# Performance work log

Hardware: AMD Instinct MI355X
Metric: run time of the kernel (lower is better)

Reference implementation:

```python
import jax, jax.numpy as jnp
import numpy as np

N_NODES = 50000
N_EDGES = 1600000
D_IN = 512
D_HEAD = 64
N_HEADS_L1 = 4


def _segment_mean(data, seg_ids, num_segments, counts):
    s = jax.ops.segment_sum(data, seg_ids, num_segments=num_segments)
    denom = jnp.maximum(counts, 1.0)
    return jnp.where(counts[:, None] > 0, s / denom[:, None], 0.0)


def setup_inputs() -> dict:
    key = jax.random.key(0)
    k1, k2, k3, k4 = jax.random.split(key, 4)
    node_features = jax.random.normal(k1, (N_NODES, D_IN), dtype=jnp.float32)
    edge_index = jax.random.randint(k2, (2, N_EDGES), 0, N_NODES, dtype=jnp.int32)
    W1 = jax.random.normal(k3, (N_HEADS_L1, D_IN, D_HEAD), dtype=jnp.float32) * (1.0 / np.sqrt(D_IN))
    W2 = jax.random.normal(k4, (N_HEADS_L1 * D_HEAD, D_HEAD), dtype=jnp.float32) * (1.0 / np.sqrt(N_HEADS_L1 * D_HEAD))
    return {"node_features": node_features, "edge_index": edge_index, "W1": W1, "W2": W2}


def reference(node_features, edge_index, W1, W2):
    n = node_features.shape[0]
    src = edge_index[0]  # segment ids (destination of aggregation in TF code)
    dst = edge_index[1]  # gathered neighbors
    counts = jax.ops.segment_sum(jnp.ones_like(src, dtype=node_features.dtype), src, num_segments=n)

    # Layer 1: 4 heads, Dense(64, no bias) -> gather(dst) -> unsorted_segment_mean(src) -> concat -> elu
    head_outs = []
    for i in range(N_HEADS_L1):
        t = node_features @ W1[i]                 # (N, 64)
        agg = _segment_mean(t[dst], src, n, counts)  # (N, 64)
        head_outs.append(agg)
    h = jax.nn.elu(jnp.concatenate(head_outs, axis=-1))  # (N, 256)

    # Layer 2: 1 head, linear activation
    t2 = h @ W2                                   # (N, 64)
    out = _segment_mean(t2[dst], src, n, counts)  # (N, 64)
    return out
```

## Files before the change

kernel.cpp:

```cpp
#include <hip/hip_runtime.h>
#include <hip/hip_bf16.h>
#include <stdint.h>

#define N_NODES 50000
#define N_EDGES 1600000
#define D_IN    512
#define D_H1    256
#define D_OUT   64

#define NBUK    196
#define MAXB    9216
#define EPB     4096
#define NPB     391
#define SLOT    96

#define NR      50001
#define ZROW    50000

typedef __attribute__((ext_vector_type(8))) short  short8;
typedef __attribute__((ext_vector_type(4))) float  f32x4;
typedef __attribute__((ext_vector_type(2))) float  f32x2;
typedef __attribute__((ext_vector_type(4))) unsigned int u32x4;
typedef __attribute__((ext_vector_type(2))) unsigned int u32x2;

typedef __attribute__((address_space(1))) void GASV;
typedef __attribute__((address_space(3))) void LASV;

static __device__ __forceinline__ unsigned short f2bf(float f) {
    union { float f; unsigned int u; } c; c.f = f;
    unsigned int u = c.u;
    return (unsigned short)((u + 0x7FFFu + ((u >> 16) & 1u)) >> 16);
}
static __device__ __forceinline__ unsigned int cvtpk(float a, float b) {
    unsigned int r;
    asm("v_cvt_pk_bf16_f32 %0, %1, %2" : "=v"(r) : "v"(a), "v"(b));
    return r;
}
static __device__ __forceinline__ unsigned short f2bf1(float f) {
    return (unsigned short)cvtpk(f, f);
}
static __device__ __forceinline__ float uasf(unsigned int u) {
    union { unsigned int u; float f; } c; c.u = u; return c.f;
}

static __device__ __forceinline__ void waitvm(int n) {
    switch (n) {
    case 0: asm volatile("s_waitcnt vmcnt(0)" ::: "memory"); break;
    case 1: asm volatile("s_waitcnt vmcnt(1)" ::: "memory"); break;
    case 2: asm volatile("s_waitcnt vmcnt(2)" ::: "memory"); break;
    case 3: asm volatile("s_waitcnt vmcnt(3)" ::: "memory"); break;
    case 4: asm volatile("s_waitcnt vmcnt(4)" ::: "memory"); break;
    case 5: asm volatile("s_waitcnt vmcnt(5)" ::: "memory"); break;
    case 6: asm volatile("s_waitcnt vmcnt(6)" ::: "memory"); break;
    default: asm volatile("s_waitcnt vmcnt(7)" ::: "memory"); break;
    }
    __builtin_amdgcn_sched_barrier(0);
}


__global__ __launch_bounds__(256) void part_kernel(const int* __restrict__ src,
                                                   const int* __restrict__ dst,
                                                   int* __restrict__ gcnt,
                                                   unsigned int* __restrict__ gbuk) {
    __shared__ int hist[NBUK];
    __shared__ int lofs[NBUK];
    __shared__ int gbase[NBUK];
    __shared__ int sbuf[256];
    __shared__ unsigned int sorted[EPB];
    __shared__ unsigned char bid[EPB];

    const int t  = threadIdx.x;
    const int e0 = blockIdx.x * EPB;
    int ec = N_EDGES - e0; if (ec > EPB) ec = EPB;

    for (int i = t; i < NBUK; i += 256) hist[i] = 0;
    __syncthreads();

    unsigned int rec[16];
    int bb[16], idx[16];
#pragma unroll
    for (int j = 0; j < 16; ++j) {
        int i = j * 256 + t;
        if (i < ec) {
            int s = src[e0 + i], d = dst[e0 + i];
            int b = s >> 8;
            rec[j] = ((unsigned int)(s & 255) << 16) | (unsigned int)d;
            bb[j]  = b;
            idx[j] = atomicAdd(&hist[b], 1);
        } else bb[j] = -1;
    }
    __syncthreads();

    int v = (t < NBUK) ? hist[t] : 0;
    sbuf[t] = v;
    __syncthreads();
#pragma unroll
    for (int off = 1; off < 256; off <<= 1) {
        int x = (t >= off) ? sbuf[t - off] : 0;
        __syncthreads();
        sbuf[t] += x;
        __syncthreads();
    }
    if (t < NBUK) {
        lofs[t]  = sbuf[t] - v;
        gbase[t] = atomicAdd(&gcnt[t], v);
    }
    __syncthreads();

#pragma unroll
    for (int j = 0; j < 16; ++j) {
        if (bb[j] >= 0) {
            int p = lofs[bb[j]] + idx[j];
            sorted[p] = rec[j];
            bid[p] = (unsigned char)bb[j];
        }
    }
    __syncthreads();

    for (int i = t; i < ec; i += 256) {
        int b = bid[i];
        int p = gbase[b] + (i - lofs[b]);
        gbuk[(size_t)b * MAXB + p] = sorted[i];
    }
}


__global__ __launch_bounds__(256) void sort_kernel(const int* __restrict__ gcnt,
                                                   const unsigned int* __restrict__ gbuk,
                                                   unsigned short* __restrict__ sdst,
                                                   int* __restrict__ deg) {
    __shared__ int hist[256];
    __shared__ int nofs[256];
    __shared__ int sbuf[256];
    __shared__ unsigned short list[MAXB];

    const int t = threadIdx.x;
    const int b = blockIdx.x;
    const int cnt = gcnt[b];
    const unsigned int* buk = gbuk + (size_t)b * MAXB;

    hist[t] = 0;
    __syncthreads();
    for (int i = t; i < cnt; i += 256)
        atomicAdd(&hist[buk[i] >> 16], 1);
    __syncthreads();

    int v = hist[t];
    sbuf[t] = v;
    __syncthreads();
#pragma unroll
    for (int off = 1; off < 256; off <<= 1) {
        int x = (t >= off) ? sbuf[t - off] : 0;
        __syncthreads();
        sbuf[t] += x;
        __syncthreads();
    }
    nofs[t] = sbuf[t] - v;
    const int n = b * 256 + t;
    if (n < N_NODES) deg[n] = v;
    __syncthreads();

    for (int i = t; i < cnt; i += 256) {
        unsigned int r = buk[i];
        int p = atomicAdd(&nofs[r >> 16], 1);
        list[p] = (unsigned short)(r & 0xffffu);
    }
    __syncthreads();

    for (int base = 0; base < 256; base += 32) {
        int node = base + (t >> 3);
        int l8   = t & 7;
        int vv   = hist[node];
        int beg  = nofs[node] - vv;
        int n2   = b * 256 + node;
        if (n2 < N_NODES) {
            int words = ((vv + 3) & ~3) >> 1;
            unsigned int* out32 = (unsigned int*)(sdst + (size_t)n2 * SLOT);
            for (int j2 = l8; j2 < words; j2 += 8) {
                unsigned int lo = (2 * j2     < vv) ? list[beg + 2 * j2]     : (unsigned int)ZROW;
                unsigned int hi = (2 * j2 + 1 < vv) ? list[beg + 2 * j2 + 1] : (unsigned int)ZROW;
                out32[j2] = lo | (hi << 16);
            }
        }
    }
}


__global__ void convw_kernel(const float* __restrict__ W1, const float* __restrict__ W2,
                             unsigned short* __restrict__ Bt1, unsigned short* __restrict__ Bt2,
                             unsigned short* __restrict__ t1, unsigned short* __restrict__ t2) {
    int i = blockIdx.x * 256 + threadIdx.x;
    if (i < 4 * 512 * 64) {
        int h = i >> 15;
        int k = (i >> 6) & 511;
        int j = i & 63;
        Bt1[(h * 64 + j) * 512 + k] = f2bf(W1[i]);
    } else if (i < 4 * 512 * 64 + 256 * 64) {
        int r = i - 4 * 512 * 64;
        int k = r >> 6;
        int n = r & 63;
        Bt2[n * 256 + k] = f2bf(W2[r]);
    } else {
        int r = i - (4 * 512 * 64 + 256 * 64);
        if (r < 8 * 32) {
            t1[(size_t)(r >> 5) * ((size_t)NR * 32) + (size_t)ZROW * 32 + (r & 31)] = 0;
        } else if (r < 8 * 32 + 2 * 32) {
            int q = r - 8 * 32;
            t2[(size_t)(q >> 5) * ((size_t)NR * 32) + (size_t)ZROW * 32 + (q & 31)] = 0;
        }
    }
}


__global__ __launch_bounds__(512) void gemm1_kernel(const float* __restrict__ A,
                                                    const unsigned short* __restrict__ Bt,
                                                    unsigned short* __restrict__ C) {
    constexpr int BM = 128, BK = 32, LDK = 40, K = D_IN, M = N_NODES;
    __shared__ unsigned short As[BM * LDK];
    __shared__ unsigned short Bs[256 * LDK];

    const int tid  = threadIdx.x;
    const int lane = tid & 63;
    const int w    = tid >> 6;
    const int wm   = (w >> 2) * 64;
    const int wn   = (w & 3) * 64;
    const int quad = lane >> 4;
    const int l15  = lane & 15;
    const int bm   = blockIdx.x;

    f32x4 acc[4][4];
#pragma unroll
    for (int mi = 0; mi < 4; ++mi)
#pragma unroll
        for (int ni = 0; ni < 4; ++ni)
            acc[mi][ni] = (f32x4){0.f, 0.f, 0.f, 0.f};

    const int r0 = tid >> 2;
    const int f8 = tid & 3;

    for (int k0 = 0; k0 < K; k0 += BK) {
        {
            int grow = bm * BM + r0;
            if (grow >= M) grow = M - 1;
            const float* ap = A + (size_t)grow * K + k0 + f8 * 8;
            f32x4 v0 = *(const f32x4*)ap;
            f32x4 v1 = *(const f32x4*)(ap + 4);
            u32x4 pk;
            pk[0] = cvtpk(v0[0], v0[1]);
            pk[1] = cvtpk(v0[2], v0[3]);
            pk[2] = cvtpk(v1[0], v1[1]);
            pk[3] = cvtpk(v1[2], v1[3]);
            *(u32x4*)&As[r0 * LDK + f8 * 8] = pk;
        }
        {
#pragma unroll
            for (int p = 0; p < 2; ++p) {
                int row = p * 128 + r0;
                u32x4 v = *(const u32x4*)(Bt + (size_t)row * K + k0 + f8 * 8);
                *(u32x4*)&Bs[row * LDK + f8 * 8] = v;
            }
        }
        __syncthreads();

        short8 af[4], bfr[4];
#pragma unroll
        for (int mi = 0; mi < 4; ++mi)
            af[mi] = *(const short8*)&As[(wm + mi * 16 + l15) * LDK + quad * 8];
#pragma unroll
        for (int ni = 0; ni < 4; ++ni)
            bfr[ni] = *(const short8*)&Bs[(wn + ni * 16 + l15) * LDK + quad * 8];
#pragma unroll
        for (int mi = 0; mi < 4; ++mi)
#pragma unroll
            for (int ni = 0; ni < 4; ++ni)
                acc[mi][ni] = __builtin_amdgcn_mfma_f32_16x16x32_bf16(af[mi], bfr[ni], acc[mi][ni], 0, 0, 0);
        __syncthreads();
    }

#pragma unroll
    for (int mi = 0; mi < 4; ++mi) {
        int row0 = bm * BM + wm + mi * 16 + quad * 4;
#pragma unroll
        for (int ni = 0; ni < 4; ++ni) {
            int col = wn + ni * 16 + l15;
            unsigned short* cp = C + (size_t)(col >> 5) * ((size_t)NR * 32) + (col & 31);
#pragma unroll
            for (int r = 0; r < 4; ++r) {
                int row = row0 + r;
                if (row < M) cp[(size_t)row * 32] = f2bf1(acc[mi][ni][r]);
            }
        }
    }
}


__global__ __launch_bounds__(256) void gemm2_kernel(const unsigned short* __restrict__ A,
                                                    const unsigned short* __restrict__ Bt,
                                                    unsigned short* __restrict__ C) {
    constexpr int BM = 64, BK = 32, LDK = 40, K = D_H1, M = N_NODES;
    __shared__ unsigned short As[BM * LDK];
    __shared__ unsigned short Bs[64 * LDK];

    const int tid  = threadIdx.x;
    const int lane = tid & 63;
    const int w    = tid >> 6;
    const int wm   = (w >> 1) * 32;
    const int wn   = (w & 1) * 32;
    const int quad = lane >> 4;
    const int l15  = lane & 15;
    const int bm   = blockIdx.x;

    f32x4 acc[2][2];
#pragma unroll
    for (int mi = 0; mi < 2; ++mi)
#pragma unroll
        for (int ni = 0; ni < 2; ++ni)
            acc[mi][ni] = (f32x4){0.f, 0.f, 0.f, 0.f};

    for (int k0 = 0; k0 < K; k0 += BK) {
        {
            int f8 = tid & 3;
            int r0 = tid >> 2;
            int grow = bm * BM + r0;
            if (grow >= M) grow = M - 1;
            u32x4 v = *(const u32x4*)(A + (size_t)grow * K + k0 + f8 * 8);
            *(u32x4*)&As[r0 * LDK + f8 * 8] = v;
        }
        {
            int f8 = tid & 3;
            int r0 = tid >> 2;
            u32x4 v = *(const u32x4*)(Bt + (size_t)r0 * K + k0 + f8 * 8);
            *(u32x4*)&Bs[r0 * LDK + f8 * 8] = v;
        }
        __syncthreads();

        short8 af[2], bfr[2];
#pragma unroll
        for (int mi = 0; mi < 2; ++mi)
            af[mi] = *(const short8*)&As[(wm + mi * 16 + l15) * LDK + quad * 8];
#pragma unroll
        for (int ni = 0; ni < 2; ++ni)
            bfr[ni] = *(const short8*)&Bs[(wn + ni * 16 + l15) * LDK + quad * 8];
#pragma unroll
        for (int mi = 0; mi < 2; ++mi)
#pragma unroll
            for (int ni = 0; ni < 2; ++ni)
                acc[mi][ni] = __builtin_amdgcn_mfma_f32_16x16x32_bf16(af[mi], bfr[ni], acc[mi][ni], 0, 0, 0);
        __syncthreads();
    }

#pragma unroll
    for (int mi = 0; mi < 2; ++mi) {
        int row0 = bm * BM + wm + mi * 16 + quad * 4;
#pragma unroll
        for (int ni = 0; ni < 2; ++ni) {
            int col = wn + ni * 16 + l15;
            unsigned short* cp = C + (size_t)(col >> 5) * ((size_t)NR * 32) + (col & 31);
#pragma unroll
            for (int r = 0; r < 4; ++r) {
                int row = row0 + r;
                if (row < M) cp[(size_t)row * 32] = f2bf1(acc[mi][ni][r]);
            }
        }
    }
}


#define AGG_ISSUE(J, B, NJ)                                                             \
    int NJ;                                                                             \
    {                                                                                   \
        const int nq4   = (end##J + 3) >> 2;                       \
        const int nfull = nq4 >> 2;                         \
        const int tq    = nq4 & 3;                               \
        int r16[4];                                                                     \
        _Pragma("unroll")                                                               \
        for (int k = 0; k < 4; ++k)                                                     \
            r16[k] = __shfl(elv##J, ((k << 4) + (lane >> 2)) & 63);                     \
        const int rtail = __shfl(elv##J, ((nfull << 4) + (lane >> 2)) & 63);            \
        for (int k = 0; k < nfull; ++k)                                                 \
            __builtin_amdgcn_global_load_lds(                                           \
                (GASV*)(tb32 + ((unsigned)r16[k] << 4) + ((lane & 3) << 2)),            \
                (LASV*)(&ring[w][B][k << 8]), 16, 0, 0);                                \
        if (lane < (tq << 4))                                                           \
            __builtin_amdgcn_global_load_lds(                                           \
                (GASV*)(tb32 + ((unsigned)rtail << 4) + ((lane & 3) << 2)),             \
                (LASV*)(&ring[w][B][nfull << 8]), 16, 0, 0);                            \
        NJ = nfull + (tq ? 1 : 0);                                                      \
    }

#define AGG_CONSUME(J, B)                                                               \
    {                                                                                   \
        const int nq = (end##J + 3) >> 2;                                               \
        f32x2 Acc = {0.f, 0.f};                                                         \
        const unsigned int* rb = &ring[w][B][lane];                                     \
        for (int q = 0; q < nq; ++q) {                                                  \
            unsigned int v = rb[q << 6];                                                \
            Acc.x += uasf(v << 16);                                                     \
            Acc.y += uasf(v & 0xffff0000u);                                             \
        }                                                                               \
        f32x2 Bv;                                                                       \
        Bv.x = __shfl_xor(Acc.x, 16); Bv.y = __shfl_xor(Acc.y, 16); Acc += Bv;          \
        Bv.x = __shfl_xor(Acc.x, 32); Bv.y = __shfl_xor(Acc.y, 32); Acc += Bv;          \
        if (lane < 16) {                                                                \
            float iv = (end##J > 0) ? (1.0f / (float)end##J) : 0.f;                     \
            float m0 = Acc.x * iv, m1 = Acc.y * iv;                                     \
            if (ELU) {                                                                  \
                m0 = (m0 > 0.f) ? m0 : (__expf(m0) - 1.f);                              \
                m1 = (m1 > 0.f) ? m1 : (__expf(m1) - 1.f);                              \
                *(unsigned int*)&hout[(size_t)(s0 + J) * D_H1 + slice * 32 + (lane & 15) * 2] = cvtpk(m0, m1); \
            } else {                                                                    \
                f32x2 r; r.x = m0; r.y = m1;                                            \
                *(f32x2*)(fout + (size_t)(s0 + J) * D_OUT + slice * 32 + (lane & 15) * 2) = r; \
            }                                                                           \
        }                                                                               \
        __builtin_amdgcn_sched_barrier(0);                                              \
    }

template<int LOGS, bool ELU>
__global__ __launch_bounds__(256) void agg_kernel(const unsigned short* __restrict__ t,
                                                  const int* __restrict__ deg,
                                                  const unsigned short* __restrict__ sdst,
                                                  unsigned short* __restrict__ hout,
                                                  float* __restrict__ fout) {
    __shared__ __align__(16) unsigned int ring[4][2][1024];
    const int bi    = blockIdx.x;
    const int slice = bi & ((1 << LOGS) - 1);
    const int g     = bi >> LOGS;
    const int w     = __builtin_amdgcn_readfirstlane(threadIdx.x >> 6);
    const int lane  = threadIdx.x & 63;
    const unsigned int* tb32 = (const unsigned int*)t + (size_t)slice * ((size_t)NR * 16);

    const int s0 = g * 16 + w * 4;
    const int end0 = deg[s0 + 0], end1 = deg[s0 + 1], end2 = deg[s0 + 2], end3 = deg[s0 + 3];
    const int elv0 = sdst[(size_t)(s0 + 0) * SLOT + lane];
    const int elv1 = sdst[(size_t)(s0 + 1) * SLOT + lane];
    const int elv2 = sdst[(size_t)(s0 + 2) * SLOT + lane];
    const int elv3 = sdst[(size_t)(s0 + 3) * SLOT + lane];

    AGG_ISSUE(0, 0, n0i);
    AGG_ISSUE(1, 1, n1i); waitvm(n1i);
    AGG_CONSUME(0, 0);
    AGG_ISSUE(2, 0, n2i); waitvm(n2i + 1);
    AGG_CONSUME(1, 1);
    AGG_ISSUE(3, 1, n3i); waitvm(n3i + 1);
    AGG_CONSUME(2, 0);
    waitvm(1);
    AGG_CONSUME(3, 1);
}


extern "C" void kernel_launch(void* const* d_in, const int* in_sizes, int n_in,
                              void* d_out, int out_size, void* d_ws, size_t ws_size,
                              hipStream_t stream) {
    const float* X  = (const float*)d_in[0];
    const int*   ei = (const int*)d_in[1];
    const float* W1 = (const float*)d_in[2];
    const float* W2 = (const float*)d_in[3];
    const int* src = ei;
    const int* dst = ei + N_EDGES;

    char* ws = (char*)d_ws;
    size_t off = 0;
    auto alloc = [&](size_t bytes) {
        off = (off + 255) & ~(size_t)255;
        void* p = ws + off;
        off += bytes;
        return p;
    };
    int*          gcnt = (int*)alloc((size_t)NBUK * 4);
    unsigned int* gbuk = (unsigned int*)alloc((size_t)NBUK * MAXB * 4);
    unsigned short* sdst = (unsigned short*)alloc(((size_t)N_NODES * SLOT + 64) * 2);
    int*          deg  = (int*)alloc((size_t)N_NODES * 4);
    unsigned short* Bt1 = (unsigned short*)alloc((size_t)D_H1 * D_IN * 2);
    unsigned short* Bt2 = (unsigned short*)alloc((size_t)D_OUT * D_H1 * 2);
    unsigned short* t1  = (unsigned short*)alloc((size_t)8 * NR * 32 * 2);
    unsigned short* h   = (unsigned short*)alloc((size_t)N_NODES * D_H1 * 2);
    unsigned short* t2  = (unsigned short*)alloc((size_t)2 * NR * 32 * 2);

    hipMemsetAsync(gcnt, 0, (size_t)NBUK * 4, stream);

    part_kernel<<<NPB, 256, 0, stream>>>(src, dst, gcnt, gbuk);
    sort_kernel<<<NBUK, 256, 0, stream>>>(gcnt, gbuk, sdst, deg);
    convw_kernel<<<(4 * 512 * 64 + 256 * 64 + 8 * 32 + 2 * 32 + 255) / 256, 256, 0, stream>>>(
        W1, W2, Bt1, Bt2, t1, t2);

    gemm1_kernel<<<(N_NODES + 127) / 128, 512, 0, stream>>>(X, Bt1, t1);
    agg_kernel<3, true><<<(N_NODES / 16) * 8, 256, 0, stream>>>(t1, deg, sdst, h, nullptr);
    gemm2_kernel<<<(N_NODES + 63) / 64, 256, 0, stream>>>(h, Bt2, t2);
    agg_kernel<1, false><<<(N_NODES / 16) * 2, 256, 0, stream>>>(t2, deg, sdst, nullptr, (float*)d_out);
}
```

Baseline: 370.5 us.

## Fuse layer-1 aggregation with layer-2 GEMM and switch to row-major t1/t2

Replaces the sliced column-major t1/t2 layout with row-major rows, so each gathered neighbour row is one contiguous 512-byte (t1) or 128-byte (t2) load. A new aggf kernel averages a whole 256-wide row per node, applies ELU, keeps h in LDS and multiplies it by W2 with MFMA in the same block. This removes the h round trip and the separate gemm2 launch. Layer-2 aggregation gets its own kernel with a chunked double-buffered pipeline, and sdst padding is rounded up to multiples of 8 so those chunks are full. In exchange the whole neighbour loop runs serially in fewer blocks with a deeper per-node pipeline, which may lower occupancy and latency hiding.

```diff
diff --git a/kernel.cpp b/kernel.cpp
--- a/kernel.cpp
+++ b/kernel.cpp
@@ -42,19 +42,8 @@
 static __device__ __forceinline__ float uasf(unsigned int u) {
     union { unsigned int u; float f; } c; c.u = u; return c.f;
 }
-
-static __device__ __forceinline__ void waitvm(int n) {
-    switch (n) {
-    case 0: asm volatile("s_waitcnt vmcnt(0)" ::: "memory"); break;
-    case 1: asm volatile("s_waitcnt vmcnt(1)" ::: "memory"); break;
-    case 2: asm volatile("s_waitcnt vmcnt(2)" ::: "memory"); break;
-    case 3: asm volatile("s_waitcnt vmcnt(3)" ::: "memory"); break;
-    case 4: asm volatile("s_waitcnt vmcnt(4)" ::: "memory"); break;
-    case 5: asm volatile("s_waitcnt vmcnt(5)" ::: "memory"); break;
-    case 6: asm volatile("s_waitcnt vmcnt(6)" ::: "memory"); break;
-    default: asm volatile("s_waitcnt vmcnt(7)" ::: "memory"); break;
-    }
-    __builtin_amdgcn_sched_barrier(0);
+static __device__ __forceinline__ void glds16(const unsigned int* g, unsigned int* l) {
+    __builtin_amdgcn_global_load_lds((GASV*)g, (LASV*)l, 16, 0, 0);
 }
 
 
@@ -174,7 +163,7 @@
         int beg  = nofs[node] - vv;
         int n2   = b * 256 + node;
         if (n2 < N_NODES) {
-            int words = ((vv + 3) & ~3) >> 1;
+            int words = ((vv + 7) & ~7) >> 1;
             unsigned int* out32 = (unsigned int*)(sdst + (size_t)n2 * SLOT);
             for (int j2 = l8; j2 < words; j2 += 8) {
                 unsigned int lo = (2 * j2     < vv) ? list[beg + 2 * j2]     : (unsigned int)ZROW;
@@ -202,11 +191,10 @@
         Bt2[n * 256 + k] = f2bf(W2[r]);
     } else {
         int r = i - (4 * 512 * 64 + 256 * 64);
-        if (r < 8 * 32) {
-            t1[(size_t)(r >> 5) * ((size_t)NR * 32) + (size_t)ZROW * 32 + (r & 31)] = 0;
-        } else if (r < 8 * 32 + 2 * 32) {
-            int q = r - 8 * 32;
-            t2[(size_t)(q >> 5) * ((size_t)NR * 32) + (size_t)ZROW * 32 + (q & 31)] = 0;
+        if (r < 256) {
+            t1[(size_t)ZROW * 256 + r] = 0;
+        } else if (r < 256 + 64) {
+            t2[(size_t)ZROW * 64 + (r - 256)] = 0;
         }
     }
 }
@@ -283,169 +271,182 @@
 #pragma unroll
         for (int ni = 0; ni < 4; ++ni) {
             int col = wn + ni * 16 + l15;
-            unsigned short* cp = C + (size_t)(col >> 5) * ((size_t)NR * 32) + (col & 31);
 #pragma unroll
             for (int r = 0; r < 4; ++r) {
                 int row = row0 + r;
-                if (row < M) cp[(size_t)row * 32] = f2bf1(acc[mi][ni][r]);
+                if (row < M) C[(size_t)row * 256 + col] = f2bf1(acc[mi][ni][r]);
             }
         }
     }
 }
 
 
-__global__ __launch_bounds__(256) void gemm2_kernel(const unsigned short* __restrict__ A,
-                                                    const unsigned short* __restrict__ Bt,
-                                                    unsigned short* __restrict__ C) {
-    constexpr int BM = 64, BK = 32, LDK = 40, K = D_H1, M = N_NODES;
-    __shared__ unsigned short As[BM * LDK];
-    __shared__ unsigned short Bs[64 * LDK];
-
-    const int tid  = threadIdx.x;
-    const int lane = tid & 63;
-    const int w    = tid >> 6;
-    const int wm   = (w >> 1) * 32;
-    const int wn   = (w & 1) * 32;
-    const int quad = lane >> 4;
-    const int l15  = lane & 15;
-    const int bm   = blockIdx.x;
-
-    f32x4 acc[2][2];
-#pragma unroll
-    for (int mi = 0; mi < 2; ++mi)
-#pragma unroll
-        for (int ni = 0; ni < 2; ++ni)
-            acc[mi][ni] = (f32x4){0.f, 0.f, 0.f, 0.f};
-
-    for (int k0 = 0; k0 < K; k0 += BK) {
-        {
-            int f8 = tid & 3;
-            int r0 = tid >> 2;
-            int grow = bm * BM + r0;
-            if (grow >= M) grow = M - 1;
-            u32x4 v = *(const u32x4*)(A + (size_t)grow * K + k0 + f8 * 8);
-            *(u32x4*)&As[r0 * LDK + f8 * 8] = v;
-        }
-        {
-            int f8 = tid & 3;
-            int r0 = tid >> 2;
-            u32x4 v = *(const u32x4*)(Bt + (size_t)r0 * K + k0 + f8 * 8);
-            *(u32x4*)&Bs[r0 * LDK + f8 * 8] = v;
-        }
-        __syncthreads();
-
-        short8 af[2], bfr[2];
-#pragma unroll
-        for (int mi = 0; mi < 2; ++mi)
-            af[mi] = *(const short8*)&As[(wm + mi * 16 + l15) * LDK + quad * 8];
-#pragma unroll
-        for (int ni = 0; ni < 2; ++ni)
-            bfr[ni] = *(const short8*)&Bs[(wn + ni * 16 + l15) * LDK + quad * 8];
-#pragma unroll
-        for (int mi = 0; mi < 2; ++mi)
-#pragma unroll
-            for (int ni = 0; ni < 2; ++ni)
-                acc[mi][ni] = __builtin_amdgcn_mfma_f32_16x16x32_bf16(af[mi], bfr[ni], acc[mi][ni], 0, 0, 0);
-        __syncthreads();
-    }
-
-#pragma unroll
-    for (int mi = 0; mi < 2; ++mi) {
-        int row0 = bm * BM + wm + mi * 16 + quad * 4;
-#pragma unroll
-        for (int ni = 0; ni < 2; ++ni) {
-            int col = wn + ni * 16 + l15;
-            unsigned short* cp = C + (size_t)(col >> 5) * ((size_t)NR * 32) + (col & 31);
-#pragma unroll
-            for (int r = 0; r < 4; ++r) {
-                int row = row0 + r;
-                if (row < M) cp[(size_t)row * 32] = f2bf1(acc[mi][ni][r]);
-            }
-        }
-    }
-}
-
-
-#define AGG_ISSUE(J, B, NJ)                                                             \
-    int NJ;                                                                             \
-    {                                                                                   \
-        const int nq4   = (end##J + 3) >> 2;                       \
-        const int nfull = nq4 >> 2;                         \
-        const int tq    = nq4 & 3;                               \
-        int r16[4];                                                                     \
-        _Pragma("unroll")                                                               \
-        for (int k = 0; k < 4; ++k)                                                     \
-            r16[k] = __shfl(elv##J, ((k << 4) + (lane >> 2)) & 63);                     \
-        const int rtail = __shfl(elv##J, ((nfull << 4) + (lane >> 2)) & 63);            \
-        for (int k = 0; k < nfull; ++k)                                                 \
-            __builtin_amdgcn_global_load_lds(                                           \
-                (GASV*)(tb32 + ((unsigned)r16[k] << 4) + ((lane & 3) << 2)),            \
-                (LASV*)(&ring[w][B][k << 8]), 16, 0, 0);                                \
-        if (lane < (tq << 4))                                                           \
-            __builtin_amdgcn_global_load_lds(                                           \
-                (GASV*)(tb32 + ((unsigned)rtail << 4) + ((lane & 3) << 2)),             \
-                (LASV*)(&ring[w][B][nfull << 8]), 16, 0, 0);                            \
-        NJ = nfull + (tq ? 1 : 0);                                                      \
-    }
-
-#define AGG_CONSUME(J, B)                                                               \
-    {                                                                                   \
-        const int nq = (end##J + 3) >> 2;                                               \
-        f32x2 Acc = {0.f, 0.f};                                                         \
-        const unsigned int* rb = &ring[w][B][lane];                                     \
-        for (int q = 0; q < nq; ++q) {                                                  \
-            unsigned int v = rb[q << 6];                                                \
-            Acc.x += uasf(v << 16);                                                     \
-            Acc.y += uasf(v & 0xffff0000u);                                             \
-        }                                                                               \
-        f32x2 Bv;                                                                       \
-        Bv.x = __shfl_xor(Acc.x, 16); Bv.y = __shfl_xor(Acc.y, 16); Acc += Bv;          \
-        Bv.x = __shfl_xor(Acc.x, 32); Bv.y = __shfl_xor(Acc.y, 32); Acc += Bv;          \
-        if (lane < 16) {                                                                \
-            float iv = (end##J > 0) ? (1.0f / (float)end##J) : 0.f;                     \
-            float m0 = Acc.x * iv, m1 = Acc.y * iv;                                     \
-            if (ELU) {                                                                  \
-                m0 = (m0 > 0.f) ? m0 : (__expf(m0) - 1.f);                              \
-                m1 = (m1 > 0.f) ? m1 : (__expf(m1) - 1.f);                              \
-                *(unsigned int*)&hout[(size_t)(s0 + J) * D_H1 + slice * 32 + (lane & 15) * 2] = cvtpk(m0, m1); \
-            } else {                                                                    \
-                f32x2 r; r.x = m0; r.y = m1;                                            \
-                *(f32x2*)(fout + (size_t)(s0 + J) * D_OUT + slice * 32 + (lane & 15) * 2) = r; \
-            }                                                                           \
-        }                                                                               \
-        __builtin_amdgcn_sched_barrier(0);                                              \
-    }
-
-template<int LOGS, bool ELU>
-__global__ __launch_bounds__(256) void agg_kernel(const unsigned short* __restrict__ t,
-                                                  const int* __restrict__ deg,
-                                                  const unsigned short* __restrict__ sdst,
-                                                  unsigned short* __restrict__ hout,
-                                                  float* __restrict__ fout) {
+__global__ __launch_bounds__(256) void aggf_kernel(const unsigned short* __restrict__ t1,
+                                                   const int* __restrict__ deg,
+                                                   const unsigned short* __restrict__ sdst,
+                                                   const unsigned short* __restrict__ Bt2,
+                                                   unsigned short* __restrict__ t2) {
     __shared__ __align__(16) unsigned int ring[4][2][1024];
-    const int bi    = blockIdx.x;
-    const int slice = bi & ((1 << LOGS) - 1);
-    const int g     = bi >> LOGS;
-    const int w     = __builtin_amdgcn_readfirstlane(threadIdx.x >> 6);
-    const int lane  = threadIdx.x & 63;
-    const unsigned int* tb32 = (const unsigned int*)t + (size_t)slice * ((size_t)NR * 16);
-
-    const int s0 = g * 16 + w * 4;
+    __shared__ __align__(16) unsigned short h_lds[16][264];
+
+    const int w    = __builtin_amdgcn_readfirstlane(threadIdx.x >> 6);
+    const int lane = threadIdx.x & 63;
+    const int s0b  = blockIdx.x * 16;
+    const int s0   = s0b + w * 4;
+    const unsigned int* tb32 = (const unsigned int*)t1;
+    const unsigned int loff = ((unsigned)(lane & 31)) << 2;
+
     const int end0 = deg[s0 + 0], end1 = deg[s0 + 1], end2 = deg[s0 + 2], end3 = deg[s0 + 3];
     const int elv0 = sdst[(size_t)(s0 + 0) * SLOT + lane];
     const int elv1 = sdst[(size_t)(s0 + 1) * SLOT + lane];
     const int elv2 = sdst[(size_t)(s0 + 2) * SLOT + lane];
     const int elv3 = sdst[(size_t)(s0 + 3) * SLOT + lane];
-
-    AGG_ISSUE(0, 0, n0i);
-    AGG_ISSUE(1, 1, n1i); waitvm(n1i);
-    AGG_CONSUME(0, 0);
-    AGG_ISSUE(2, 0, n2i); waitvm(n2i + 1);
-    AGG_CONSUME(1, 1);
-    AGG_ISSUE(3, 1, n3i); waitvm(n3i + 1);
-    AGG_CONSUME(2, 0);
-    waitvm(1);
-    AGG_CONSUME(3, 1);
+    asm volatile("" :: "v"(end0), "v"(end1), "v"(end2), "v"(end3),
+                       "v"(elv0), "v"(elv1), "v"(elv2), "v"(elv3));
+
+#define AGGF_ISSUE(ELV, C, B)                                                           \
+    {                                                                                   \
+        int q  = ((C) << 3) + (lane >> 5);                                              \
+        int ra = __shfl(ELV, q);                                                        \
+        int rb_ = __shfl(ELV, q + 2);                                                   \
+        int rc = __shfl(ELV, q + 4);                                                    \
+        int rd = __shfl(ELV, q + 6);                                                    \
+        unsigned int* dp = &ring[w][B][0];                                              \
+        glds16(tb32 + (unsigned)ra  * 128u + loff, dp);                                 \
+        glds16(tb32 + (unsigned)rb_ * 128u + loff, dp + 256);                           \
+        glds16(tb32 + (unsigned)rc  * 128u + loff, dp + 512);                           \
+        glds16(tb32 + (unsigned)rd  * 128u + loff, dp + 768);                           \
+    }
+
+#define AGGF_CONSUME(B)                                                                 \
+    {                                                                                   \
+        const unsigned int* rbp = &ring[w][B][lane << 1];                               \
+        _Pragma("unroll")                                                               \
+        for (int r = 0; r < 8; ++r) {                                                   \
+            u32x2 v = *(const u32x2*)(rbp + (r << 7));                                  \
+            a0 += uasf(v[0] << 16); a1 += uasf(v[0] & 0xffff0000u);                     \
+            a2 += uasf(v[1] << 16); a3 += uasf(v[1] & 0xffff0000u);                     \
+        }                                                                               \
+    }
+
+#define AGGF_NODE(J)                                                                    \
+    {                                                                                   \
+        const int end = end##J;                                                         \
+        const int nch = ((end + 7) & ~7) >> 3;                                          \
+        float a0 = 0.f, a1 = 0.f, a2 = 0.f, a3 = 0.f;                                   \
+        if (nch > 0) {                                                                  \
+            AGGF_ISSUE(elv##J, 0, 0);                                                   \
+            for (int c = 1; c < nch; ++c) {                                             \
+                AGGF_ISSUE(elv##J, c, c & 1);                                           \
+                asm volatile("s_waitcnt vmcnt(4)" ::: "memory");                        \
+                __builtin_amdgcn_sched_barrier(0);                                      \
+                AGGF_CONSUME((c - 1) & 1);                                              \
+            }                                                                           \
+            asm volatile("s_waitcnt vmcnt(0)" ::: "memory");                            \
+            __builtin_amdgcn_sched_barrier(0);                                          \
+            AGGF_CONSUME((nch - 1) & 1);                                                \
+        }                                                                               \
+        float iv = (end > 0) ? (1.0f / (float)end) : 0.f;                               \
+        float m0 = a0 * iv, m1 = a1 * iv, m2 = a2 * iv, m3 = a3 * iv;                   \
+        m0 = (m0 > 0.f) ? m0 : (__expf(m0) - 1.f);                                      \
+        m1 = (m1 > 0.f) ? m1 : (__expf(m1) - 1.f);                                      \
+        m2 = (m2 > 0.f) ? m2 : (__expf(m2) - 1.f);                                      \
+        m3 = (m3 > 0.f) ? m3 : (__expf(m3) - 1.f);                                      \
+        u32x2 hw;                                                                       \
+        hw[0] = cvtpk(m0, m1);                                                          \
+        hw[1] = cvtpk(m2, m3);                                                          \
+        *(u32x2*)&h_lds[(w << 2) + J][lane << 2] = hw;                                  \
+    }
+
+    AGGF_NODE(0);
+    AGGF_NODE(1);
+    AGGF_NODE(2);
+    AGGF_NODE(3);
+
+    __syncthreads();
+
+    {
+        const int l15 = lane & 15, quad = lane >> 4;
+        f32x4 acc = (f32x4){0.f, 0.f, 0.f, 0.f};
+#pragma unroll
+        for (int st = 0; st < 8; ++st) {
+            short8 afr = *(const short8*)&h_lds[l15][st * 32 + quad * 8];
+            short8 bfr = *(const short8*)(Bt2 + (size_t)(w * 16 + l15) * 256 + st * 32 + quad * 8);
+            acc = __builtin_amdgcn_mfma_f32_16x16x32_bf16(afr, bfr, acc, 0, 0, 0);
+        }
+#pragma unroll
+        for (int r = 0; r < 4; ++r)
+            t2[(size_t)(s0b + quad * 4 + r) * 64 + w * 16 + l15] = f2bf1(acc[r]);
+    }
+}
+
+
+__global__ __launch_bounds__(256) void agg2_kernel(const unsigned short* __restrict__ t2,
+                                                   const int* __restrict__ deg,
+                                                   const unsigned short* __restrict__ sdst,
+                                                   float* __restrict__ out) {
+    __shared__ __align__(16) unsigned int ring[4][2][256];
+
+    const int w    = __builtin_amdgcn_readfirstlane(threadIdx.x >> 6);
+    const int lane = threadIdx.x & 63;
+    const int s0   = blockIdx.x * 16 + w * 4;
+    const unsigned int* tb32 = (const unsigned int*)t2;
+    const unsigned int loff = ((unsigned)(lane & 7)) << 2;
+
+    const int end0 = deg[s0 + 0], end1 = deg[s0 + 1], end2 = deg[s0 + 2], end3 = deg[s0 + 3];
+    const int elv0 = sdst[(size_t)(s0 + 0) * SLOT + lane];
+    const int elv1 = sdst[(size_t)(s0 + 1) * SLOT + lane];
+    const int elv2 = sdst[(size_t)(s0 + 2) * SLOT + lane];
+    const int elv3 = sdst[(size_t)(s0 + 3) * SLOT + lane];
+    asm volatile("" :: "v"(end0), "v"(end1), "v"(end2), "v"(end3),
+                       "v"(elv0), "v"(elv1), "v"(elv2), "v"(elv3));
+
+#define AGG2_ISSUE(ELV, D, B)                                                           \
+    {                                                                                   \
+        int r = __shfl(ELV, ((D) << 3) + (lane >> 3));                                  \
+        glds16(tb32 + (unsigned)r * 32u + loff, &ring[w][B][0]);                        \
+    }
+
+#define AGG2_CONSUME(B)                                                                 \
+    {                                                                                   \
+        const unsigned int* rbp = &ring[w][B][lane & 31];                               \
+        _Pragma("unroll")                                                               \
+        for (int i = 0; i < 4; ++i) {                                                   \
+            unsigned int v = rbp[(((i << 1) + (lane >> 5)) << 5)];                      \
+            a0 += uasf(v << 16); a1 += uasf(v & 0xffff0000u);                           \
+        }                                                                               \
+    }
+
+#define AGG2_NODE(J)                                                                    \
+    {                                                                                   \
+        const int end = end##J;                                                         \
+        const int nch = ((end + 7) & ~7) >> 3;                                          \
+        float a0 = 0.f, a1 = 0.f;                                                       \
+        if (nch > 0) {                                                                  \
+            AGG2_ISSUE(elv##J, 0, 0);                                                   \
+            for (int d = 1; d < nch; ++d) {                                             \
+                AGG2_ISSUE(elv##J, d, d & 1);                                           \
+                asm volatile("s_waitcnt vmcnt(1)" ::: "memory");                        \
+                __builtin_amdgcn_sched_barrier(0);                                      \
+                AGG2_CONSUME((d - 1) & 1);                                              \
+            }                                                                           \
+            asm volatile("s_waitcnt vmcnt(0)" ::: "memory");                            \
+            __builtin_amdgcn_sched_barrier(0);                                          \
+            AGG2_CONSUME((nch - 1) & 1);                                                \
+        }                                                                               \
+        a0 += __shfl_xor(a0, 32);                                                       \
+        a1 += __shfl_xor(a1, 32);                                                       \
+        if (lane < 32) {                                                                \
+            float iv = (end > 0) ? (1.0f / (float)end) : 0.f;                           \
+            f32x2 rr; rr.x = a0 * iv; rr.y = a1 * iv;                                   \
+            *(f32x2*)(out + (size_t)(s0 + J) * D_OUT + (lane & 31) * 2) = rr;           \
+        }                                                                               \
+    }
+
+    AGG2_NODE(0);
+    AGG2_NODE(1);
+    AGG2_NODE(2);
+    AGG2_NODE(3);
 }
 
 
@@ -473,19 +474,17 @@
     int*          deg  = (int*)alloc((size_t)N_NODES * 4);
     unsigned short* Bt1 = (unsigned short*)alloc((size_t)D_H1 * D_IN * 2);
     unsigned short* Bt2 = (unsigned short*)alloc((size_t)D_OUT * D_H1 * 2);
-    unsigned short* t1  = (unsigned short*)alloc((size_t)8 * NR * 32 * 2);
-    unsigned short* h   = (unsigned short*)alloc((size_t)N_NODES * D_H1 * 2);
-    unsigned short* t2  = (unsigned short*)alloc((size_t)2 * NR * 32 * 2);
+    unsigned short* t1  = (unsigned short*)alloc((size_t)NR * D_H1 * 2);
+    unsigned short* t2  = (unsigned short*)alloc((size_t)NR * D_OUT * 2);
 
     hipMemsetAsync(gcnt, 0, (size_t)NBUK * 4, stream);
 
     part_kernel<<<NPB, 256, 0, stream>>>(src, dst, gcnt, gbuk);
     sort_kernel<<<NBUK, 256, 0, stream>>>(gcnt, gbuk, sdst, deg);
-    convw_kernel<<<(4 * 512 * 64 + 256 * 64 + 8 * 32 + 2 * 32 + 255) / 256, 256, 0, stream>>>(
+    convw_kernel<<<(4 * 512 * 64 + 256 * 64 + 256 + 64 + 255) / 256, 256, 0, stream>>>(
         W1, W2, Bt1, Bt2, t1, t2);
 
     gemm1_kernel<<<(N_NODES + 127) / 128, 512, 0, stream>>>(X, Bt1, t1);
-    agg_kernel<3, true><<<(N_NODES / 16) * 8, 256, 0, stream>>>(t1, deg, sdst, h, nullptr);
-    gemm2_kernel<<<(N_NODES + 63) / 64, 256, 0, stream>>>(h, Bt2, t2);
-    agg_kernel<1, false><<<(N_NODES / 16) * 2, 256, 0, stream>>>(t2, deg, sdst, nullptr, (float*)d_out);
-}
+    aggf_kernel<<<N_NODES / 16, 256, 0, stream>>>(t1, deg, sdst, Bt2, t2);
+    agg2_kernel<<<N_NODES / 16, 256, 0, stream>>>(t2, deg, sdst, (float*)d_out);
+}
```

Result: faster. 351.7 us (-5.0%).
